# Performance work log

Measured on AMD Instinct MI355X. Metric: run time of the kernel, lower is better.

The kernel has to match this reference:

```python
import jax, jax.numpy as jnp
import numpy as np

NUM_HEADS = 16
TOP_K = 6


def setup_inputs() -> dict:
    key = jax.random.key(0)
    ks = jax.random.split(key, 16)
    B, P = 8192, 4096
    QD = PD = D = 1024  # query_dim, prototype_dim, token_dim
    s = lambda d: 1.0 / np.sqrt(d)
    return {
        "query": jax.random.normal(ks[0], (B, QD), jnp.float32),
        "prototype_bank": jax.random.normal(ks[1], (P, PD), jnp.float32),
        "prototype_logits": jax.random.normal(ks[2], (B, P), jnp.float32),
        # query_proj / prototype_proj (torch Linear: y = x @ W.T + b)
        "Wq_proj": jax.random.normal(ks[3], (D, QD), jnp.float32) * s(QD),
        "bq_proj": jnp.zeros((D,), jnp.float32),
        "Wp_proj": jax.random.normal(ks[4], (D, PD), jnp.float32) * s(PD),
        "bp_proj": jnp.zeros((D,), jnp.float32),
        # MultiheadAttention in-proj (q, k, v) and out-proj
        "Wq": jax.random.normal(ks[5], (D, D), jnp.float32) * s(D),
        "bq": jnp.zeros((D,), jnp.float32),
        "Wk": jax.random.normal(ks[6], (D, D), jnp.float32) * s(D),
        "bk": jnp.zeros((D,), jnp.float32),
        "Wv": jax.random.normal(ks[7], (D, D), jnp.float32) * s(D),
        "bv": jnp.zeros((D,), jnp.float32),
        "Wo": jax.random.normal(ks[8], (D, D), jnp.float32) * s(D),
        "bo": jnp.zeros((D,), jnp.float32),
    }


def reference(query, prototype_bank, prototype_logits,
              Wq_proj, bq_proj, Wp_proj, bp_proj,
              Wq, bq, Wk, bk, Wv, bv, Wo, bo):
    B, D = query.shape[0], Wq.shape[0]
    h = NUM_HEADS
    dh = D // h
    k = min(TOP_K, prototype_bank.shape[0])

    # top-k prototype selection (indices only)
    _, topk_idx = jax.lax.top_k(prototype_logits, k)            # [B, k]

    projected_bank = prototype_bank @ Wp_proj.T + bp_proj        # [P, D]
    selected = projected_bank[topk_idx]                          # [B, k, D]

    attn_query = (query @ Wq_proj.T + bq_proj)[:, None, :]       # [B, 1, D]

    # MultiheadAttention (batch_first, eval mode so dropout is a no-op)
    qh = (attn_query @ Wq.T + bq).reshape(B, 1, h, dh).transpose(0, 2, 1, 3)  # [B,h,1,dh]
    kh = (selected @ Wk.T + bk).reshape(B, k, h, dh).transpose(0, 2, 1, 3)    # [B,h,k,dh]
    vh = (selected @ Wv.T + bv).reshape(B, k, h, dh).transpose(0, 2, 1, 3)    # [B,h,k,dh]

    scores = jnp.einsum("bhqd,bhkd->bhqk", qh, kh) / jnp.sqrt(jnp.float32(dh))
    w = jax.nn.softmax(scores, axis=-1)                          # [B,h,1,k]
    ctx = jnp.einsum("bhqk,bhkd->bhqd", w, vh)                   # [B,h,1,dh]
    ctx = ctx.transpose(0, 2, 1, 3).reshape(B, 1, D)
    context = ctx @ Wo.T + bo                                    # [B,1,D]

    attn_weights = w.mean(axis=1)                                # avg heads -> [B,1,k]
    return context[:, 0, :], attn_weights[:, 0, :]
```

## Files before the change

### kernel.cpp

```cpp
#include <hip/hip_runtime.h>
#include <stdint.h>

#define B_ROWS 8192
#define P_ROWS 4096
#define D_DIM  1024
#define K_TOP  6

typedef __attribute__((ext_vector_type(8))) short short8;
typedef __attribute__((ext_vector_type(4))) float floatx4;

static __device__ __forceinline__ float bf2f(unsigned short h) {
  return __uint_as_float(((unsigned)h) << 16);
}
static __device__ __forceinline__ unsigned short f2bf(float f) {
  unsigned u = __float_as_uint(f);
  u += 0x7FFFu + ((u >> 16) & 1u);
  return (unsigned short)(u >> 16);
}

typedef __attribute__((address_space(3))) unsigned int lds32_t;
typedef const __attribute__((address_space(1))) unsigned int g32_t;

static __device__ __forceinline__ void gld_lds16(const unsigned short* g, unsigned short* l) {
  __builtin_amdgcn_global_load_lds((g32_t*)(uintptr_t)g,
                                   (lds32_t*)(unsigned int)(uintptr_t)l, 16, 0, 0);
}

template <bool OUT_BF16, bool HAS_BIAS>
static __device__ __forceinline__ void gemm_bt_body(
    const unsigned short* __restrict__ A, const unsigned short* __restrict__ Bw,
    const float* __restrict__ bias, void* __restrict__ Cout, int m0, int n0) {
  constexpr int Kd = 1024, Nd = 1024, BK = 64;
  __shared__ unsigned short sA[128 * BK];
  __shared__ unsigned short sB[128 * BK];

  const int tid = threadIdx.x;
  const int wid = tid >> 6, lane = tid & 63;
  const int wm = (wid & 1) * 64, wn = (wid >> 1) * 64;

  floatx4 acc[4][4];
#pragma unroll
  for (int mt = 0; mt < 4; ++mt)
#pragma unroll
    for (int nt = 0; nt < 4; ++nt) acc[mt][nt] = (floatx4){0.f, 0.f, 0.f, 0.f};

  const int ld_row = lane >> 3;
  const int ld_col = (lane & 7) * 8;

  for (int kt = 0; kt < Kd / BK; ++kt) {
    const int k0 = kt * BK;
    __syncthreads();
#pragma unroll
    for (int c = 0; c < 4; ++c) {
      const int ch = wid * 4 + c;
      const int r = ch * 8 + ld_row;
      gld_lds16(A  + (size_t)(m0 + r) * Kd + k0 + ld_col, sA + ch * 512);
      gld_lds16(Bw + (size_t)(n0 + r) * Kd + k0 + ld_col, sB + ch * 512);
    }
    __syncthreads();
#pragma unroll
    for (int ks = 0; ks < 2; ++ks) {
      const int kk = ks * 32 + (lane >> 4) * 8;
      short8 a[4], b[4];
#pragma unroll
      for (int t = 0; t < 4; ++t) {
        a[t] = *(const short8*)(sA + (wm + t * 16 + (lane & 15)) * BK + kk);
        b[t] = *(const short8*)(sB + (wn + t * 16 + (lane & 15)) * BK + kk);
      }
#pragma unroll
      for (int mt = 0; mt < 4; ++mt)
#pragma unroll
        for (int nt = 0; nt < 4; ++nt)
          acc[mt][nt] = __builtin_amdgcn_mfma_f32_16x16x32_bf16(a[mt], b[nt], acc[mt][nt], 0, 0, 0);
    }
  }

  const int er = lane >> 4;
  const int ec = lane & 15;
#pragma unroll
  for (int mt = 0; mt < 4; ++mt) {
#pragma unroll
    for (int nt = 0; nt < 4; ++nt) {
      const int col = n0 + wn + nt * 16 + ec;
      const float bv = HAS_BIAS ? bias[col] : 0.f;
#pragma unroll
      for (int r = 0; r < 4; ++r) {
        const int row = m0 + wm + mt * 16 + er * 4 + r;
        const float v = acc[mt][nt][r] + bv;
        if (OUT_BF16)
          ((unsigned short*)Cout)[(size_t)row * Nd + col] = f2bf(v);
        else
          ((float*)Cout)[(size_t)row * Nd + col] = v;
      }
    }
  }
}

template <bool OUT_BF16>
__global__ __launch_bounds__(256) void gemm_bt_kernel(
    const unsigned short* __restrict__ A, const unsigned short* __restrict__ Bw,
    const float* __restrict__ bias, void* __restrict__ Cout) {
  gemm_bt_body<OUT_BF16, true>(A, Bw, bias, Cout, blockIdx.y * 128, blockIdx.x * 128);
}

static __device__ __forceinline__ void cswap64(unsigned long long& hi, unsigned long long& lo) {
  unsigned long long x = hi, y = lo;
  bool c = y > x;
  hi = c ? y : x;
  lo = c ? x : y;
}

#define PREP_BLOCKS 19712
struct PrepArgs {
  const float* cs[6]; unsigned short* cd[6];
  const float* ts[2]; unsigned short* td[2];
  const float* bW[3]; const float* bp[3]; const float* bb[3]; float* bo[3];
  const float* logits; int* topk;
};

__global__ __launch_bounds__(256) void prep_kernel(PrepArgs a) {
  const int b0 = blockIdx.x;
  if (b0 < 2048) {
    const int wid = threadIdx.x >> 6;
    const int lane = threadIdx.x & 63;
    const int row = b0 * 4 + wid;
    const float4* lp4 = (const float4*)(a.logits + (size_t)row * P_ROWS);

    unsigned long long m0 = 0, m1 = 0, m2 = 0, m3 = 0, m4 = 0, m5 = 0;
    auto ins = [&](float val, int idx) {
      unsigned u = __float_as_uint(val);
      u ^= ((unsigned)((int)u >> 31)) | 0x80000000u;
      unsigned long long key =
          (((unsigned long long)u) << 32) | (unsigned long long)(0xFFFFFFFFu - (unsigned)idx);
      m5 = key > m5 ? key : m5;
      cswap64(m4, m5);
      cswap64(m3, m4);
      cswap64(m2, m3);
      cswap64(m1, m2);
      cswap64(m0, m1);
    };
#pragma unroll
    for (int j = 0; j < 16; ++j) {
      float4 v = lp4[j * 64 + lane];
      const int base = j * 256 + lane * 4;
      ins(v.x, base);
      ins(v.y, base + 1);
      ins(v.z, base + 2);
      ins(v.w, base + 3);
    }
#pragma unroll
    for (int it = 0; it < K_TOP; ++it) {
      unsigned long long best = m0;
#pragma unroll
      for (int o = 32; o > 0; o >>= 1) {
        unsigned long long t = __shfl_xor(best, o);
        best = t > best ? t : best;
      }
      if (lane == 0)
        a.topk[row * K_TOP + it] = (int)(0xFFFFFFFFu - (unsigned)(best & 0xFFFFFFFFull));
      const bool pred = (m0 == best);
      m0 = pred ? m1 : m0;
      m1 = pred ? m2 : m1;
      m2 = pred ? m3 : m2;
      m3 = pred ? m4 : m3;
      m4 = pred ? m5 : m4;
      m5 = pred ? 0ull : m5;
    }
    return;
  }
  const int b = b0 - 2048;
  if (b < 16384) {
    int seg; unsigned sb;
    if (b < 8192) { seg = 0; sb = 0; }
    else if (b < 12288) { seg = 1; sb = 8192; }
    else { seg = 2 + ((b - 12288) >> 10); sb = 12288u + (((unsigned)(seg - 2)) << 10); }
    const unsigned off = (((unsigned)b - sb) << 10) + threadIdx.x * 4u;
    float4 v = *(const float4*)(a.cs[seg] + off);
    ushort4 o;
    o.x = f2bf(v.x); o.y = f2bf(v.y); o.z = f2bf(v.z); o.w = f2bf(v.w);
    *(ushort4*)(a.cd[seg] + off) = o;
  } else if (b < 16896) {
    __shared__ unsigned short t[64][72];
    const int tt = b - 16384;
    const int which = tt >> 8;
    const int tile = tt & 255;
    const int i0 = (tile >> 4) * 64, j0 = (tile & 15) * 64;
    const float* src = a.ts[which];
    unsigned short* dst = a.td[which];
    const int r = threadIdx.x >> 4;
    const int c = (threadIdx.x & 15) * 4;
#pragma unroll
    for (int rr = 0; rr < 4; ++rr) {
      const int row = r + rr * 16;
      float4 v = *(const float4*)(src + (size_t)(i0 + row) * D_DIM + j0 + c);
      t[c + 0][row] = f2bf(v.x); t[c + 1][row] = f2bf(v.y);
      t[c + 2][row] = f2bf(v.z); t[c + 3][row] = f2bf(v.w);
    }
    __syncthreads();
#pragma unroll
    for (int rr = 0; rr < 4; ++rr) {
      const int row = r + rr * 16;
      ushort4 v = *(const ushort4*)(&t[row][c]);
      *(ushort4*)(dst + (size_t)(j0 + row) * D_DIM + i0 + c) = v;
    }
  } else {
    const int b3 = b - 16896;
    const int j = b3 >> 8;
    const int nb = b3 & 255;
    const int wid = threadIdx.x >> 6, lane = threadIdx.x & 63;
    const int n = nb * 4 + wid;
    const float* W = a.bW[j] + (size_t)n * D_DIM;
    const float* p = a.bp[j];
    float s = 0.f;
#pragma unroll
    for (int d = lane; d < D_DIM; d += 64) s += W[d] * p[d];
#pragma unroll
    for (int o = 32; o > 0; o >>= 1) s += __shfl_xor(s, o);
    if (lane == 0) a.bo[j][n] = s + a.bb[j][n];
  }
}

#define MID_BLOCKS 192
struct MidArgs {
  const unsigned short* fA[3]; const unsigned short* fW[3]; unsigned short* fC[3];
};

__global__ __launch_bounds__(256) void mid_kernel(MidArgs a) {
  const int z = blockIdx.x >> 6;
  const int tile = blockIdx.x & 63;
  gemm_bt_body<true, false>(a.fA[z], a.fW[z], nullptr, (void*)a.fC[z],
                            (tile >> 3) * 128, (tile & 7) * 128);
}

#define GEMM3_BLOCKS 1024
struct Gemm3Args {
  const unsigned short* A[3]; const unsigned short* W[3]; const float* bias[3];
  unsigned short* C[3];
};

__global__ __launch_bounds__(256) void gemm3_kernel(Gemm3Args a) {
  const int b = blockIdx.x;
  int seg, lb;
  if (b < 512) { seg = 0; lb = b; }
  else if (b < 768) { seg = 1; lb = b - 512; }
  else { seg = 2; lb = b - 768; }
  gemm_bt_body<true, true>(a.A[seg], a.W[seg], a.bias[seg], (void*)a.C[seg],
                           (lb >> 3) * 128, (lb & 7) * 128);
}

__global__ __launch_bounds__(256) void attn_kernel(
    const unsigned short* __restrict__ q2,
    const unsigned short* __restrict__ kb,
    const unsigned short* __restrict__ vb,
    const int* __restrict__ topk,
    unsigned short* __restrict__ ctx,
    float* __restrict__ attnw) {
  const int b = blockIdx.x;
  const int wid = threadIdx.x >> 6, lane = threadIdx.x & 63;
  __shared__ float wsum[4][K_TOP];

  int idx[K_TOP];
#pragma unroll
  for (int j = 0; j < K_TOP; ++j) idx[j] = topk[b * K_TOP + j];

  float hw[K_TOP] = {0.f, 0.f, 0.f, 0.f, 0.f, 0.f};
#pragma unroll
  for (int hh = 0; hh < 4; ++hh) {
    const int h = wid * 4 + hh;
    const int off = h * 64 + lane;
    const float qv = bf2f(q2[(size_t)b * D_DIM + off]);
    float s[K_TOP];
#pragma unroll
    for (int j = 0; j < K_TOP; ++j)
      s[j] = qv * bf2f(kb[(size_t)idx[j] * D_DIM + off]);
#pragma unroll
    for (int j = 0; j < K_TOP; ++j)
#pragma unroll
      for (int o = 32; o > 0; o >>= 1) s[j] += __shfl_xor(s[j], o);

    float mx = -1e30f;
#pragma unroll
    for (int j = 0; j < K_TOP; ++j) mx = fmaxf(mx, s[j] * 0.125f);
    float e[K_TOP], sum = 0.f;
#pragma unroll
    for (int j = 0; j < K_TOP; ++j) { e[j] = __expf(s[j] * 0.125f - mx); sum += e[j]; }
    const float inv = 1.0f / sum;

    float o = 0.f;
#pragma unroll
    for (int j = 0; j < K_TOP; ++j) {
      const float w = e[j] * inv;
      hw[j] += w;
      o += w * bf2f(vb[(size_t)idx[j] * D_DIM + off]);
    }
    ctx[(size_t)b * D_DIM + off] = f2bf(o);
  }
  if (lane == 0) {
#pragma unroll
    for (int j = 0; j < K_TOP; ++j) wsum[wid][j] = hw[j];
  }
  __syncthreads();
  if (threadIdx.x < K_TOP) {
    const float t = wsum[0][threadIdx.x] + wsum[1][threadIdx.x] +
                    wsum[2][threadIdx.x] + wsum[3][threadIdx.x];
    attnw[(size_t)b * K_TOP + threadIdx.x] = t * (1.0f / 16.0f);
  }
}

extern "C" void kernel_launch(void* const* d_in, const int* in_sizes, int n_in,
                              void* d_out, int out_size, void* d_ws, size_t ws_size,
                              hipStream_t stream) {
  const float* query   = (const float*)d_in[0];
  const float* bank    = (const float*)d_in[1];
  const float* logits  = (const float*)d_in[2];
  const float* Wq_proj = (const float*)d_in[3];
  const float* bq_proj = (const float*)d_in[4];
  const float* Wp_proj = (const float*)d_in[5];
  const float* bp_proj = (const float*)d_in[6];
  const float* Wq      = (const float*)d_in[7];
  const float* bq      = (const float*)d_in[8];
  const float* Wk      = (const float*)d_in[9];
  const float* bk      = (const float*)d_in[10];
  const float* Wv      = (const float*)d_in[11];
  const float* bv      = (const float*)d_in[12];
  const float* Wo      = (const float*)d_in[13];
  const float* bo      = (const float*)d_in[14];

  char* ws = (char*)d_ws;
  size_t off = 0;
  auto alloc = [&](size_t bytes) {
    void* p = ws + off;
    off += (bytes + 255) & ~(size_t)255;
    return p;
  };
  unsigned short* q_bf    = (unsigned short*)alloc((size_t)B_ROWS * D_DIM * 2);
  unsigned short* bank_bf = (unsigned short*)alloc((size_t)P_ROWS * D_DIM * 2);
  unsigned short* q2_bf   = (unsigned short*)alloc((size_t)B_ROWS * D_DIM * 2);
  unsigned short* kb_bf   = (unsigned short*)alloc((size_t)P_ROWS * D_DIM * 2);
  unsigned short* vb_bf   = (unsigned short*)alloc((size_t)P_ROWS * D_DIM * 2);
  unsigned short* wq_bf   = (unsigned short*)alloc((size_t)D_DIM * D_DIM * 2);
  unsigned short* wk_bf   = (unsigned short*)alloc((size_t)D_DIM * D_DIM * 2);
  unsigned short* wv_bf   = (unsigned short*)alloc((size_t)D_DIM * D_DIM * 2);
  unsigned short* wo_bf   = (unsigned short*)alloc((size_t)D_DIM * D_DIM * 2);
  unsigned short* wqpT_bf = (unsigned short*)alloc((size_t)D_DIM * D_DIM * 2);
  unsigned short* wppT_bf = (unsigned short*)alloc((size_t)D_DIM * D_DIM * 2);
  unsigned short* wcq_bf  = (unsigned short*)alloc((size_t)D_DIM * D_DIM * 2);
  unsigned short* wck_bf  = (unsigned short*)alloc((size_t)D_DIM * D_DIM * 2);
  unsigned short* wcv_bf  = (unsigned short*)alloc((size_t)D_DIM * D_DIM * 2);
  float* bcq              = (float*)alloc(D_DIM * 4);
  float* bck              = (float*)alloc(D_DIM * 4);
  float* bcv              = (float*)alloc(D_DIM * 4);
  int* topk               = (int*)alloc((size_t)B_ROWS * K_TOP * 4);

  float* out_ctx  = (float*)d_out;
  float* out_attn = out_ctx + (size_t)B_ROWS * D_DIM;
  (void)out_ctx;

  PrepArgs pa;
  pa.cs[0] = query; pa.cd[0] = q_bf;
  pa.cs[1] = bank;  pa.cd[1] = bank_bf;
  pa.cs[2] = Wq;    pa.cd[2] = wq_bf;
  pa.cs[3] = Wk;    pa.cd[3] = wk_bf;
  pa.cs[4] = Wv;    pa.cd[4] = wv_bf;
  pa.cs[5] = Wo;    pa.cd[5] = wo_bf;
  pa.ts[0] = Wq_proj; pa.td[0] = wqpT_bf;
  pa.ts[1] = Wp_proj; pa.td[1] = wppT_bf;
  pa.bW[0] = Wq; pa.bp[0] = bq_proj; pa.bb[0] = bq; pa.bo[0] = bcq;
  pa.bW[1] = Wk; pa.bp[1] = bp_proj; pa.bb[1] = bk; pa.bo[1] = bck;
  pa.bW[2] = Wv; pa.bp[2] = bp_proj; pa.bb[2] = bv; pa.bo[2] = bcv;
  pa.logits = logits; pa.topk = topk;
  prep_kernel<<<PREP_BLOCKS, 256, 0, stream>>>(pa);

  MidArgs ma;
  ma.fA[0] = wq_bf; ma.fW[0] = wqpT_bf; ma.fC[0] = wcq_bf;
  ma.fA[1] = wk_bf; ma.fW[1] = wppT_bf; ma.fC[1] = wck_bf;
  ma.fA[2] = wv_bf; ma.fW[2] = wppT_bf; ma.fC[2] = wcv_bf;
  mid_kernel<<<MID_BLOCKS, 256, 0, stream>>>(ma);

  Gemm3Args ga;
  ga.A[0] = q_bf;    ga.W[0] = wcq_bf; ga.bias[0] = bcq; ga.C[0] = q2_bf;
  ga.A[1] = bank_bf; ga.W[1] = wck_bf; ga.bias[1] = bck; ga.C[1] = kb_bf;
  ga.A[2] = bank_bf; ga.W[2] = wcv_bf; ga.bias[2] = bcv; ga.C[2] = vb_bf;
  gemm3_kernel<<<GEMM3_BLOCKS, 256, 0, stream>>>(ga);

  attn_kernel<<<B_ROWS, 256, 0, stream>>>(q2_bf, kb_bf, vb_bf, topk, q_bf, out_attn);

  dim3 grid2(D_DIM / 128, B_ROWS / 128);
  gemm_bt_kernel<false><<<grid2, 256, 0, stream>>>(q_bf, wo_bf, bo, d_out);
}
```

Measured before the change: 435.5 us.

## Use threshold filtering for top-k selection instead of per-element insertion sort

Top-k selection per row now loads all logits into registers and finds a threshold, the 6th-largest per-lane maximum across the wave. It then compacts only values at or above that threshold into shared memory and selects the top 6 from at most 64 candidates by wave reductions. This replaces the per-element 64-bit compare-swap insertion into a six-entry list, cutting ALU work in the logits pass. If more than 64 candidates pass, it falls back to the original insertion path. It adds register pressure from holding 16 float4 values and LDS atomics.

```diff
diff --git a/kernel.cpp b/kernel.cpp
--- a/kernel.cpp
+++ b/kernel.cpp
@@ -110,6 +110,12 @@
   lo = c ? x : y;
 }
 
+static __device__ __forceinline__ unsigned long long topk_key(float val, int idx) {
+  unsigned u = __float_as_uint(val);
+  u ^= ((unsigned)((int)u >> 31)) | 0x80000000u;
+  return (((unsigned long long)u) << 32) | (unsigned long long)(0xFFFFFFFFu - (unsigned)idx);
+}
+
 #define PREP_BLOCKS 19712
 struct PrepArgs {
   const float* cs[6]; unsigned short* cd[6];
@@ -121,50 +127,95 @@
 __global__ __launch_bounds__(256) void prep_kernel(PrepArgs a) {
   const int b0 = blockIdx.x;
   if (b0 < 2048) {
+    __shared__ int s_cnt[4];
+    __shared__ unsigned long long s_cand[4][64];
     const int wid = threadIdx.x >> 6;
     const int lane = threadIdx.x & 63;
     const int row = b0 * 4 + wid;
     const float4* lp4 = (const float4*)(a.logits + (size_t)row * P_ROWS);
 
-    unsigned long long m0 = 0, m1 = 0, m2 = 0, m3 = 0, m4 = 0, m5 = 0;
-    auto ins = [&](float val, int idx) {
-      unsigned u = __float_as_uint(val);
-      u ^= ((unsigned)((int)u >> 31)) | 0x80000000u;
-      unsigned long long key =
-          (((unsigned long long)u) << 32) | (unsigned long long)(0xFFFFFFFFu - (unsigned)idx);
-      m5 = key > m5 ? key : m5;
-      cswap64(m4, m5);
-      cswap64(m3, m4);
-      cswap64(m2, m3);
-      cswap64(m1, m2);
-      cswap64(m0, m1);
-    };
+    float4 r[16];
+#pragma unroll
+    for (int j = 0; j < 16; ++j) r[j] = lp4[j * 64 + lane];
+    float mx = -1e38f;
+#pragma unroll
+    for (int j = 0; j < 16; ++j)
+      mx = fmaxf(mx, fmaxf(fmaxf(r[j].x, r[j].y), fmaxf(r[j].z, r[j].w)));
+
+    float mkeep = mx, tau = mx;
+#pragma unroll
+    for (int it = 0; it < K_TOP; ++it) {
+      float best = mkeep;
+#pragma unroll
+      for (int o = 32; o > 0; o >>= 1) best = fmaxf(best, __shfl_xor(best, o));
+      tau = best;
+      if (it < K_TOP - 1) mkeep = (mkeep == best) ? -1e38f : mkeep;
+    }
+
+    if (lane == 0) s_cnt[wid] = 0;
+
 #pragma unroll
     for (int j = 0; j < 16; ++j) {
-      float4 v = lp4[j * 64 + lane];
       const int base = j * 256 + lane * 4;
-      ins(v.x, base);
-      ins(v.y, base + 1);
-      ins(v.z, base + 2);
-      ins(v.w, base + 3);
-    }
-#pragma unroll
-    for (int it = 0; it < K_TOP; ++it) {
-      unsigned long long best = m0;
-#pragma unroll
-      for (int o = 32; o > 0; o >>= 1) {
-        unsigned long long t = __shfl_xor(best, o);
-        best = t > best ? t : best;
+      const float4 v = r[j];
+      if (v.x >= tau) { int s = atomicAdd(&s_cnt[wid], 1); if (s < 64) s_cand[wid][s] = topk_key(v.x, base); }
+      if (v.y >= tau) { int s = atomicAdd(&s_cnt[wid], 1); if (s < 64) s_cand[wid][s] = topk_key(v.y, base + 1); }
+      if (v.z >= tau) { int s = atomicAdd(&s_cnt[wid], 1); if (s < 64) s_cand[wid][s] = topk_key(v.z, base + 2); }
+      if (v.w >= tau) { int s = atomicAdd(&s_cnt[wid], 1); if (s < 64) s_cand[wid][s] = topk_key(v.w, base + 3); }
+    }
+    const int n = s_cnt[wid];
+
+    if (n <= 64) {
+      unsigned long long key = (lane < n) ? s_cand[wid][lane] : 0ull;
+#pragma unroll
+      for (int it = 0; it < K_TOP; ++it) {
+        unsigned long long best = key;
+#pragma unroll
+        for (int o = 32; o > 0; o >>= 1) {
+          unsigned long long t = __shfl_xor(best, o);
+          best = t > best ? t : best;
+        }
+        if (lane == 0)
+          a.topk[row * K_TOP + it] = (int)(0xFFFFFFFFu - (unsigned)(best & 0xFFFFFFFFull));
+        key = (key == best) ? 0ull : key;
       }
-      if (lane == 0)
-        a.topk[row * K_TOP + it] = (int)(0xFFFFFFFFu - (unsigned)(best & 0xFFFFFFFFull));
-      const bool pred = (m0 == best);
-      m0 = pred ? m1 : m0;
-      m1 = pred ? m2 : m1;
-      m2 = pred ? m3 : m2;
-      m3 = pred ? m4 : m3;
-      m4 = pred ? m5 : m4;
-      m5 = pred ? 0ull : m5;
+    } else {
+      unsigned long long m0 = 0, m1 = 0, m2 = 0, m3 = 0, m4 = 0, m5 = 0;
+      auto ins = [&](float val, int idx) {
+        unsigned long long key = topk_key(val, idx);
+        m5 = key > m5 ? key : m5;
+        cswap64(m4, m5);
+        cswap64(m3, m4);
+        cswap64(m2, m3);
+        cswap64(m1, m2);
+        cswap64(m0, m1);
+      };
+#pragma unroll
+      for (int j = 0; j < 16; ++j) {
+        const int base = j * 256 + lane * 4;
+        ins(r[j].x, base);
+        ins(r[j].y, base + 1);
+        ins(r[j].z, base + 2);
+        ins(r[j].w, base + 3);
+      }
+#pragma unroll
+      for (int it = 0; it < K_TOP; ++it) {
+        unsigned long long best = m0;
+#pragma unroll
+        for (int o = 32; o > 0; o >>= 1) {
+          unsigned long long t = __shfl_xor(best, o);
+          best = t > best ? t : best;
+        }
+        if (lane == 0)
+          a.topk[row * K_TOP + it] = (int)(0xFFFFFFFFu - (unsigned)(best & 0xFFFFFFFFull));
+        const bool pred = (m0 == best);
+        m0 = pred ? m1 : m0;
+        m1 = pred ? m2 : m1;
+        m2 = pred ? m3 : m2;
+        m3 = pred ? m4 : m3;
+        m4 = pred ? m5 : m4;
+        m5 = pred ? 0ull : m5;
+      }
     }
     return;
   }
```

Result: no change. 436.7 us (+0.3%).
